# Kernel optimization log

Measured on AMD Instinct MI355X. Metric: run time of the kernel, lower is better.

## Reference

```python
import jax, jax.numpy as jnp
import numpy as np

W_WIN = 5  # sliding rank-pooling window (init arg w)
GRAY_W = np.array([0.2989, 0.587, 0.114], dtype=np.float32)  # torchvision Grayscale


def _window_weight_matrix(T, w):
    # Wmat[t, s] = rank-pooling weight of frame s inside window starting at t.
    # Window t covers frames t..t+N-1 with N = min(w, T-t); weights 2*(j+1)-N-1.
    M = np.zeros((T, T), dtype=np.float32)
    for t in range(T):
        N = min(w, T - t)
        for j in range(N):
            M[t, t + j] = 2.0 * (j + 1) - N - 1
    return jnp.asarray(M)


def setup_inputs() -> dict:
    key = jax.random.key(0)
    x = jax.random.normal(key, (8, 3, 64, 224, 224), dtype=jnp.float32)
    return {"x": x}


def reference(x):
    B, C, T, H, W = x.shape
    Wmat = _window_weight_matrix(T, W_WIN)  # [T, T], banded (bandwidth W_WIN)
    # Weighted sum over each sliding window: re[t] = sum_s Wmat[t,s] * x[:,:,s]
    re = jnp.einsum('ts,bcshw->tbchw', Wmat, x)  # [T,B,C,H,W]
    re = jax.nn.gelu(re, approximate=False)  # torch F.gelu is exact (erf)
    # Global (over B,C,H,W) min-subtract then max-normalize, per window t
    mn = re.min(axis=(1, 2, 3, 4), keepdims=True)
    re = re - mn
    mx = re.max(axis=(1, 2, 3, 4), keepdims=True)
    denom = jnp.where(mx != 0, mx, mx + 1e-5)
    re = re / denom
    # Grayscale: ITU-R 601 weighted channel sum -> 1 channel
    gray = jnp.einsum('tbchw,c->tbhw', re, jnp.asarray(GRAY_W, re.dtype))
    out = jnp.transpose(gray, (1, 0, 2, 3))[:, None]  # [B,1,T,H,W]
    mask = jnp.zeros((B, 1, W_WIN - 1, H, W), dtype=out.dtype)
    return jnp.concatenate([mask, out], axis=2)  # [B,1,T+w-1,H,W]
```

## Files before the change

### kernel.cpp

```cpp
#include <hip/hip_runtime.h>

#define HW 50176
#define HW2 25088
#define HW4 12544
#define TT 64
#define NB1 3136
#define NB3 3808
#define SUMW 0.9999f

__device__ __forceinline__ float gelu_erf(float x) {
    return 0.5f * x * (1.0f + erff(0.70710678f * x));
}
__device__ __forceinline__ float fast_rcp(float v) {
    float r; asm("v_rcp_f32 %0, %1" : "=v"(r) : "v"(v)); return r;
}
__device__ __forceinline__ float gelu_fast(float x) {
    float x2 = x * x;
    float e = exp2f(-x * fmaf(0.1029433f, x2, 2.3022078f));
    return x * fast_rcp(1.0f + e);
}
__device__ __forceinline__ unsigned encf(float f) {
    unsigned u = __float_as_uint(f);
    return (u & 0x80000000u) ? ~u : (u | 0x80000000u);
}
__device__ __forceinline__ float decf(unsigned u) {
    unsigned b = (u & 0x80000000u) ? (u ^ 0x80000000u) : ~u;
    return __uint_as_float(b);
}
__device__ __forceinline__ unsigned pk_min_f16(unsigned a, unsigned b) {
    unsigned r; asm("v_pk_min_f16 %0, %1, %2" : "=v"(r) : "v"(a), "v"(b)); return r;
}
__device__ __forceinline__ unsigned pack2(float lo, float hi) {
    auto p = __builtin_amdgcn_cvt_pkrtz(lo, hi);
    return __builtin_bit_cast(unsigned, p);
}
__device__ __forceinline__ unsigned mm2(float2 r) {
    return pk_min_f16(pack2(r.x, -r.x), pack2(r.y, -r.y));
}
__device__ __forceinline__ float2 re_full2(float2 w0, float2 w1, float2 w3, float2 w4) {
    float2 r;
    r.x = fmaf(4.f, w4.x - w0.x, 2.f * (w3.x - w1.x));
    r.y = fmaf(4.f, w4.y - w0.y, 2.f * (w3.y - w1.y));
    return r;
}

template<bool WGS>
__global__ __launch_bounds__(256, 6) void k_pass1(const float* __restrict__ x,
                                                  unsigned* __restrict__ gmm,
                                                  unsigned* __restrict__ gs) {
    __shared__ unsigned smin[16], smax[16];
    const int tid = threadIdx.x;
    if (tid < 16) { smin[tid] = 0xFFFFFFFFu; smax[tid] = 0u; }
    __syncthreads();

    const int bid = blockIdx.x;
    const int b   = bid / 392;
    const int rem = bid - b * 392;
    const int tc  = rem / 98;
    const int hwb = rem - tc * 98;
    const int t0  = tc * 16;
    const int hw  = (hwb * 256 + tid) * 2;
    const float* xa = x + ((size_t)(b * 3 + 0) * TT + t0) * (size_t)HW + hw;
    const float* xb = x + ((size_t)(b * 3 + 1) * TT + t0) * (size_t)HW + hw;
    const float* xc = x + ((size_t)(b * 3 + 2) * TT + t0) * (size_t)HW + hw;
    unsigned* gp = gs + ((size_t)b * TT + t0) * (size_t)HW2 + (hwb * 256 + tid);

    unsigned acc[16];
    #pragma unroll
    for (int j = 0; j < 16; ++j) acc[j] = 0x7BFF7BFFu;

    #define LDA(f) (*(const float2*)(xa + (size_t)(f) * HW))
    #define LDB(f) (*(const float2*)(xb + (size_t)(f) * HW))
    #define LDC(f) (*(const float2*)(xc + (size_t)(f) * HW))

    auto step = [&](float2 ra, float2 rb, float2 rc, int j) {
        acc[j] = pk_min_f16(acc[j], pk_min_f16(pk_min_f16(mm2(ra), mm2(rb)), mm2(rc)));
        if constexpr (WGS) {
            float gx = fmaf(0.114f, gelu_fast(rc.x), fmaf(0.587f, gelu_fast(rb.x), 0.2989f * gelu_fast(ra.x)));
            float gy = fmaf(0.114f, gelu_fast(rc.y), fmaf(0.587f, gelu_fast(rb.y), 0.2989f * gelu_fast(ra.y)));
            gp[(size_t)j * HW2] = pack2(gx, gy);
        }
    };

    float2 a0 = LDA(0), a1 = LDA(1), a2 = LDA(2), a3 = LDA(3), a4 = LDA(4), pa = LDA(5);
    float2 b0 = LDB(0), b1 = LDB(1), b2 = LDB(2), b3 = LDB(3), b4 = LDB(4), pb = LDB(5);
    float2 c0 = LDC(0), c1 = LDC(1), c2 = LDC(2), c3 = LDC(3), c4 = LDC(4), pc = LDC(5);

    if (tc < 3) {
        #pragma unroll
        for (int j = 0; j < 16; ++j) {
            step(re_full2(a0, a1, a3, a4), re_full2(b0, b1, b3, b4), re_full2(c0, c1, c3, c4), j);
            a0 = a1; a1 = a2; a2 = a3; a3 = a4; a4 = pa;
            b0 = b1; b1 = b2; b2 = b3; b3 = b4; b4 = pb;
            c0 = c1; c1 = c2; c2 = c3; c3 = c4; c4 = pc;
            if (j < 14) { pa = LDA(j + 6); pb = LDB(j + 6); pc = LDC(j + 6); }
        }
    } else {
        #pragma unroll
        for (int j = 0; j < 16; ++j) {
            float2 ra, rb, rc;
            if (j < 12) {
                ra = re_full2(a0, a1, a3, a4); rb = re_full2(b0, b1, b3, b4); rc = re_full2(c0, c1, c3, c4);
            } else if (j == 12) {
                ra.x = fmaf(3.f, a3.x - a0.x, a2.x - a1.x); ra.y = fmaf(3.f, a3.y - a0.y, a2.y - a1.y);
                rb.x = fmaf(3.f, b3.x - b0.x, b2.x - b1.x); rb.y = fmaf(3.f, b3.y - b0.y, b2.y - b1.y);
                rc.x = fmaf(3.f, c3.x - c0.x, c2.x - c1.x); rc.y = fmaf(3.f, c3.y - c0.y, c2.y - c1.y);
            } else if (j == 13) {
                ra.x = 2.f*(a2.x-a0.x); ra.y = 2.f*(a2.y-a0.y);
                rb.x = 2.f*(b2.x-b0.x); rb.y = 2.f*(b2.y-b0.y);
                rc.x = 2.f*(c2.x-c0.x); rc.y = 2.f*(c2.y-c0.y);
            } else if (j == 14) {
                ra.x = a1.x-a0.x; ra.y = a1.y-a0.y;
                rb.x = b1.x-b0.x; rb.y = b1.y-b0.y;
                rc.x = c1.x-c0.x; rc.y = c1.y-c0.y;
            } else {
                ra.x = ra.y = 0.f; rb = ra; rc = ra;
            }
            step(ra, rb, rc, j);
            a0 = a1; a1 = a2; a2 = a3; a3 = a4; a4 = pa;
            b0 = b1; b1 = b2; b2 = b3; b3 = b4; b4 = pb;
            c0 = c1; c1 = c2; c2 = c3; c3 = c4; c4 = pc;
            if (j < 10) { pa = LDA(j + 6); pb = LDB(j + 6); pc = LDC(j + 6); }
        }
    }
    #undef LDA
    #undef LDB
    #undef LDC

    const int lane = tid & 63;
    unsigned keep = 0x7BFF7BFFu;
    #pragma unroll
    for (int j = 0; j < 16; ++j) {
        unsigned a = acc[j];
        #pragma unroll
        for (int off = 32; off; off >>= 1)
            a = pk_min_f16(a, (unsigned)__shfl_xor((int)a, off, 64));
        if (lane == j) keep = a;
    }

    if (lane < 16) {
        union { unsigned u; _Float16 h[2]; } cv; cv.u = keep;
        const float amin = (float)cv.h[0];
        const float amax = -(float)cv.h[1];
        const float g0 = gelu_erf(amin), g1 = gelu_erf(amax);
        const float gmax = fmaxf(g0, g1);
        const float XSTAR = -0.7517916f;
        float gmin;
        if (amin >= XSTAR)      gmin = g0;
        else if (amax <= XSTAR) gmin = g1;
        else                    gmin = fminf(gelu_erf(XSTAR), fminf(g0, g1));
        atomicMin(&smin[lane], encf(gmin));
        atomicMax(&smax[lane], encf(gmax));
    }
    __syncthreads();
    if (tid < 16)            atomicMin(&gmm[t0 + tid], smin[tid]);
    else if (tid < 32)       atomicMax(&gmm[TT + t0 + tid - 16], smax[tid - 16]);
}

__global__ __launch_bounds__(256) void k_pass3(const unsigned* __restrict__ gs,
                                               const unsigned* __restrict__ gmm,
                                               float* __restrict__ out) {
    const int bid = blockIdx.x;
    const int b   = bid / 476;
    const int r   = bid - b * 476;
    const int t   = r / 7;
    const int seg = r - t * 7;
    const int base4 = seg * 1792 + threadIdx.x;
    float4* op = (float4*)out + ((size_t)b * 68 + t) * HW4 + base4;

    if (t < 4) {
        float4 z = make_float4(0.f, 0.f, 0.f, 0.f);
        #pragma unroll
        for (int k = 0; k < 7; ++k) op[k * 256] = z;
        return;
    }
    const int tm = t - 4;
    const float mn = decf(gmm[tm]);
    const float mx = decf(gmm[TT + tm]) - mn;
    const float inv = fast_rcp((mx != 0.f) ? mx : 1e-5f);
    const float A = inv, Bv = -mn * SUMW * inv;

    const uint2* gpp = (const uint2*)gs + ((size_t)b * TT + tm) * HW4 + base4;
    #pragma unroll
    for (int k = 0; k < 7; ++k) {
        uint2 v = gpp[k * 256];
        union { unsigned u; _Float16 h[2]; } lo, hi; lo.u = v.x; hi.u = v.y;
        float4 o;
        o.x = fmaf((float)lo.h[0], A, Bv);
        o.y = fmaf((float)lo.h[1], A, Bv);
        o.z = fmaf((float)hi.h[0], A, Bv);
        o.w = fmaf((float)hi.h[1], A, Bv);
        op[k * 256] = o;
    }
}

__global__ void k_consts(const unsigned* __restrict__ gmm, float* __restrict__ ab) {
    int t = threadIdx.x;
    float mn = decf(gmm[t]);
    float mx = decf(gmm[TT + t]) - mn;
    float inv = 1.0f / ((mx != 0.0f) ? mx : 1e-5f);
    ab[t]      = inv;
    ab[TT + t] = -mn * SUMW * inv;
}

__global__ __launch_bounds__(256) void k_pass2_direct(const float* __restrict__ x,
                                                      const float* __restrict__ ab,
                                                      float* __restrict__ out) {
    __shared__ float sA[TT], sB[TT];
    const int tid = threadIdx.x;
    if (tid < TT)          sA[tid] = ab[tid];
    else if (tid < 2 * TT) sB[tid - TT] = ab[tid];
    __syncthreads();

    const int pix = blockIdx.x * 256 + tid;
    const int b  = pix / HW;
    const int hw = pix - b * HW;
    const float* x0 = x + (size_t)(b * 3) * (TT * (size_t)HW) + hw;
    const float* x1 = x0 + (size_t)TT * HW;
    const float* x2 = x1 + (size_t)TT * HW;
    float* op = out + (size_t)b * (68 * (size_t)HW) + hw;

    op[0] = 0.f; op[HW] = 0.f; op[2 * (size_t)HW] = 0.f; op[3 * (size_t)HW] = 0.f;
    op += 4 * (size_t)HW;

    float a0 = x0[0], a1 = x0[HW], a2 = x0[2*HW], a3 = x0[3*HW], a4 = x0[4*HW];
    float b0 = x1[0], b1 = x1[HW], b2 = x1[2*HW], b3 = x1[3*HW], b4 = x1[4*HW];
    float c0 = x2[0], c1 = x2[HW], c2 = x2[2*HW], c3 = x2[3*HW], c4 = x2[4*HW];

    auto emit = [&](int t, float ra, float rb, float rc) {
        float gsv = 0.2989f * gelu_erf(ra) + 0.587f * gelu_erf(rb) + 0.114f * gelu_erf(rc);
        op[(size_t)t * HW] = fmaf(gsv, sA[t], sB[t]);
    };

    for (int t = 0; t < 59; ++t) {
        emit(t, 4.f*(a4-a0) + 2.f*(a3-a1), 4.f*(b4-b0) + 2.f*(b3-b1), 4.f*(c4-c0) + 2.f*(c3-c1));
        a0=a1; a1=a2; a2=a3; a3=a4; a4 = x0[(size_t)(t+5)*HW];
        b0=b1; b1=b2; b2=b3; b3=b4; b4 = x1[(size_t)(t+5)*HW];
        c0=c1; c1=c2; c2=c3; c3=c4; c4 = x2[(size_t)(t+5)*HW];
    }
    emit(59, 4.f*(a4-a0) + 2.f*(a3-a1), 4.f*(b4-b0) + 2.f*(b3-b1), 4.f*(c4-c0) + 2.f*(c3-c1));
    a0=a1; a1=a2; a2=a3; a3=a4; b0=b1; b1=b2; b2=b3; b3=b4; c0=c1; c1=c2; c2=c3; c3=c4;
    emit(60, 3.f*(a3-a0) + (a2-a1), 3.f*(b3-b0) + (b2-b1), 3.f*(c3-c0) + (c2-c1));
    a0=a1; a1=a2; a2=a3; b0=b1; b1=b2; b2=b3; c0=c1; c1=c2; c2=c3;
    emit(61, 2.f*(a2-a0), 2.f*(b2-b0), 2.f*(c2-c0));
    a0=a1; a1=a2; b0=b1; b1=b2; c0=c1; c1=c2;
    emit(62, a1-a0, b1-b0, c1-c0);
    op[63 * (size_t)HW] = sB[63];
}

extern "C" void kernel_launch(void* const* d_in, const int* in_sizes, int n_in,
                              void* d_out, int out_size, void* d_ws, size_t ws_size,
                              hipStream_t stream) {
    const float* x = (const float*)d_in[0];
    float* out = (float*)d_out;
    unsigned* gmm = (unsigned*)d_ws;
    float* ab = (float*)d_ws + 128;
    unsigned* gs = (unsigned*)((char*)d_ws + 1024);
    const size_t need = 1024 + (size_t)8 * TT * (size_t)HW * 2;

    hipMemsetAsync(gmm, 0xFF, TT * sizeof(unsigned), stream);
    hipMemsetAsync(gmm + TT, 0x00, TT * sizeof(unsigned), stream);

    if (ws_size >= need) {
        k_pass1<true><<<NB1, 256, 0, stream>>>(x, gmm, gs);
        k_pass3<<<NB3, 256, 0, stream>>>(gs, gmm, out);
    } else {
        k_pass1<false><<<NB1, 256, 0, stream>>>(x, gmm, nullptr);
        k_consts<<<1, 64, 0, stream>>>(gmm, ab);
        k_pass2_direct<<<1568, 256, 0, stream>>>(x, ab, out);
    }
}
```

Baseline: 132.5 us.

## Process full time axis per thread with scalar pixels to remove halo reloads

```diff
diff --git a/kernel.cpp b/kernel.cpp
--- a/kernel.cpp
+++ b/kernel.cpp
@@ -1,10 +1,9 @@
 #include <hip/hip_runtime.h>
 
 #define HW 50176
-#define HW2 25088
 #define HW4 12544
 #define TT 64
-#define NB1 3136
+#define NB1 1568
 #define NB3 3808
 #define SUMW 0.9999f
 
@@ -34,127 +33,105 @@
     auto p = __builtin_amdgcn_cvt_pkrtz(lo, hi);
     return __builtin_bit_cast(unsigned, p);
 }
-__device__ __forceinline__ unsigned mm2(float2 r) {
-    return pk_min_f16(pack2(r.x, -r.x), pack2(r.y, -r.y));
-}
-__device__ __forceinline__ float2 re_full2(float2 w0, float2 w1, float2 w3, float2 w4) {
-    float2 r;
-    r.x = fmaf(4.f, w4.x - w0.x, 2.f * (w3.x - w1.x));
-    r.y = fmaf(4.f, w4.y - w0.y, 2.f * (w3.y - w1.y));
-    return r;
+__device__ __forceinline__ unsigned pk2(float r) {
+    return pack2(r, -r);
 }
 
 template<bool WGS>
 __global__ __launch_bounds__(256, 6) void k_pass1(const float* __restrict__ x,
                                                   unsigned* __restrict__ gmm,
-                                                  unsigned* __restrict__ gs) {
-    __shared__ unsigned smin[16], smax[16];
+                                                  _Float16* __restrict__ gs) {
+    __shared__ unsigned smin[TT], smax[TT];
     const int tid = threadIdx.x;
-    if (tid < 16) { smin[tid] = 0xFFFFFFFFu; smax[tid] = 0u; }
+    if (tid < TT) { smin[tid] = 0xFFFFFFFFu; smax[tid] = 0u; }
     __syncthreads();
 
-    const int bid = blockIdx.x;
-    const int b   = bid / 392;
-    const int rem = bid - b * 392;
-    const int tc  = rem / 98;
-    const int hwb = rem - tc * 98;
-    const int t0  = tc * 16;
-    const int hw  = (hwb * 256 + tid) * 2;
-    const float* xa = x + ((size_t)(b * 3 + 0) * TT + t0) * (size_t)HW + hw;
-    const float* xb = x + ((size_t)(b * 3 + 1) * TT + t0) * (size_t)HW + hw;
-    const float* xc = x + ((size_t)(b * 3 + 2) * TT + t0) * (size_t)HW + hw;
-    unsigned* gp = gs + ((size_t)b * TT + t0) * (size_t)HW2 + (hwb * 256 + tid);
-
-    unsigned acc[16];
+    const int gid = blockIdx.x * 256 + tid;
+    const int b   = gid / HW;
+    const int hw  = gid - b * HW;
+    const float* xa = x + ((size_t)(b * 3 + 0) * TT) * (size_t)HW + hw;
+    const float* xb = x + ((size_t)(b * 3 + 1) * TT) * (size_t)HW + hw;
+    const float* xc = x + ((size_t)(b * 3 + 2) * TT) * (size_t)HW + hw;
+    _Float16* gp = gs + ((size_t)b * TT) * (size_t)HW + hw;
+
+    #define LA(f) xa[(size_t)(f) * HW]
+    #define LB(f) xb[(size_t)(f) * HW]
+    #define LC(f) xc[(size_t)(f) * HW]
+
+    float a0 = LA(0), a1 = LA(1), a2 = LA(2), a3 = LA(3), a4 = LA(4), pa = LA(5), qa = LA(6);
+    float b0 = LB(0), b1 = LB(1), b2 = LB(2), b3 = LB(3), b4 = LB(4), pb = LB(5), qb = LB(6);
+    float c0 = LC(0), c1 = LC(1), c2 = LC(2), c3 = LC(3), c4 = LC(4), pc = LC(5), qc = LC(6);
+
+    const int lane = tid & 63;
+
     #pragma unroll
-    for (int j = 0; j < 16; ++j) acc[j] = 0x7BFF7BFFu;
-
-    #define LDA(f) (*(const float2*)(xa + (size_t)(f) * HW))
-    #define LDB(f) (*(const float2*)(xb + (size_t)(f) * HW))
-    #define LDC(f) (*(const float2*)(xc + (size_t)(f) * HW))
-
-    auto step = [&](float2 ra, float2 rb, float2 rc, int j) {
-        acc[j] = pk_min_f16(acc[j], pk_min_f16(pk_min_f16(mm2(ra), mm2(rb)), mm2(rc)));
-        if constexpr (WGS) {
-            float gx = fmaf(0.114f, gelu_fast(rc.x), fmaf(0.587f, gelu_fast(rb.x), 0.2989f * gelu_fast(ra.x)));
-            float gy = fmaf(0.114f, gelu_fast(rc.y), fmaf(0.587f, gelu_fast(rb.y), 0.2989f * gelu_fast(ra.y)));
-            gp[(size_t)j * HW2] = pack2(gx, gy);
+    for (int seg = 0; seg < 4; ++seg) {
+        unsigned acc[16];
+        #pragma unroll
+        for (int j = 0; j < 16; ++j) acc[j] = 0x7BFF7BFFu;
+
+        #pragma unroll
+        for (int j = 0; j < 16; ++j) {
+            const int t = seg * 16 + j;
+            float ra, rb, rc;
+            if (t < 60) {
+                ra = fmaf(4.f, a4 - a0, 2.f * (a3 - a1));
+                rb = fmaf(4.f, b4 - b0, 2.f * (b3 - b1));
+                rc = fmaf(4.f, c4 - c0, 2.f * (c3 - c1));
+            } else if (t == 60) {
+                ra = fmaf(3.f, a3 - a0, a2 - a1);
+                rb = fmaf(3.f, b3 - b0, b2 - b1);
+                rc = fmaf(3.f, c3 - c0, c2 - c1);
+            } else if (t == 61) {
+                ra = 2.f * (a2 - a0); rb = 2.f * (b2 - b0); rc = 2.f * (c2 - c0);
+            } else if (t == 62) {
+                ra = a1 - a0; rb = b1 - b0; rc = c1 - c0;
+            } else {
+                ra = rb = rc = 0.f;
+            }
+            acc[j] = pk_min_f16(acc[j], pk_min_f16(pk_min_f16(pk2(ra), pk2(rb)), pk2(rc)));
+            if constexpr (WGS) {
+                float g = fmaf(0.114f, gelu_fast(rc),
+                          fmaf(0.587f, gelu_fast(rb), 0.2989f * gelu_fast(ra)));
+                gp[(size_t)t * HW] = (_Float16)g;
+            }
+            a0 = a1; a1 = a2; a2 = a3; a3 = a4; a4 = pa; pa = qa;
+            b0 = b1; b1 = b2; b2 = b3; b3 = b4; b4 = pb; pb = qb;
+            c0 = c1; c1 = c2; c2 = c3; c3 = c4; c4 = pc; pc = qc;
+            if (t < 57) { qa = LA(t + 7); qb = LB(t + 7); qc = LC(t + 7); }
         }
-    };
-
-    float2 a0 = LDA(0), a1 = LDA(1), a2 = LDA(2), a3 = LDA(3), a4 = LDA(4), pa = LDA(5);
-    float2 b0 = LDB(0), b1 = LDB(1), b2 = LDB(2), b3 = LDB(3), b4 = LDB(4), pb = LDB(5);
-    float2 c0 = LDC(0), c1 = LDC(1), c2 = LDC(2), c3 = LDC(3), c4 = LDC(4), pc = LDC(5);
-
-    if (tc < 3) {
+
+        unsigned keep = 0x7BFF7BFFu;
         #pragma unroll
         for (int j = 0; j < 16; ++j) {
-            step(re_full2(a0, a1, a3, a4), re_full2(b0, b1, b3, b4), re_full2(c0, c1, c3, c4), j);
-            a0 = a1; a1 = a2; a2 = a3; a3 = a4; a4 = pa;
-            b0 = b1; b1 = b2; b2 = b3; b3 = b4; b4 = pb;
-            c0 = c1; c1 = c2; c2 = c3; c3 = c4; c4 = pc;
-            if (j < 14) { pa = LDA(j + 6); pb = LDB(j + 6); pc = LDC(j + 6); }
+            unsigned a = acc[j];
+            #pragma unroll
+            for (int off = 32; off; off >>= 1)
+                a = pk_min_f16(a, (unsigned)__shfl_xor((int)a, off, 64));
+            if (lane == j) keep = a;
         }
-    } else {
-        #pragma unroll
-        for (int j = 0; j < 16; ++j) {
-            float2 ra, rb, rc;
-            if (j < 12) {
-                ra = re_full2(a0, a1, a3, a4); rb = re_full2(b0, b1, b3, b4); rc = re_full2(c0, c1, c3, c4);
-            } else if (j == 12) {
-                ra.x = fmaf(3.f, a3.x - a0.x, a2.x - a1.x); ra.y = fmaf(3.f, a3.y - a0.y, a2.y - a1.y);
-                rb.x = fmaf(3.f, b3.x - b0.x, b2.x - b1.x); rb.y = fmaf(3.f, b3.y - b0.y, b2.y - b1.y);
-                rc.x = fmaf(3.f, c3.x - c0.x, c2.x - c1.x); rc.y = fmaf(3.f, c3.y - c0.y, c2.y - c1.y);
-            } else if (j == 13) {
-                ra.x = 2.f*(a2.x-a0.x); ra.y = 2.f*(a2.y-a0.y);
-                rb.x = 2.f*(b2.x-b0.x); rb.y = 2.f*(b2.y-b0.y);
-                rc.x = 2.f*(c2.x-c0.x); rc.y = 2.f*(c2.y-c0.y);
-            } else if (j == 14) {
-                ra.x = a1.x-a0.x; ra.y = a1.y-a0.y;
-                rb.x = b1.x-b0.x; rb.y = b1.y-b0.y;
-                rc.x = c1.x-c0.x; rc.y = c1.y-c0.y;
-            } else {
-                ra.x = ra.y = 0.f; rb = ra; rc = ra;
-            }
-            step(ra, rb, rc, j);
-            a0 = a1; a1 = a2; a2 = a3; a3 = a4; a4 = pa;
-            b0 = b1; b1 = b2; b2 = b3; b3 = b4; b4 = pb;
-            c0 = c1; c1 = c2; c2 = c3; c3 = c4; c4 = pc;
-            if (j < 10) { pa = LDA(j + 6); pb = LDB(j + 6); pc = LDC(j + 6); }
+        if (lane < 16) {
+            union { unsigned u; _Float16 h[2]; } cv; cv.u = keep;
+            const float amin = (float)cv.h[0];
+            const float amax = -(float)cv.h[1];
+            const float g0 = gelu_erf(amin), g1 = gelu_erf(amax);
+            const float gmax = fmaxf(g0, g1);
+            const float XSTAR = -0.7517916f;
+            float gmin;
+            if (amin >= XSTAR)      gmin = g0;
+            else if (amax <= XSTAR) gmin = g1;
+            else                    gmin = fminf(gelu_erf(XSTAR), fminf(g0, g1));
+            atomicMin(&smin[seg * 16 + lane], encf(gmin));
+            atomicMax(&smax[seg * 16 + lane], encf(gmax));
         }
     }
-    #undef LDA
-    #undef LDB
-    #undef LDC
-
-    const int lane = tid & 63;
-    unsigned keep = 0x7BFF7BFFu;
-    #pragma unroll
-    for (int j = 0; j < 16; ++j) {
-        unsigned a = acc[j];
-        #pragma unroll
-        for (int off = 32; off; off >>= 1)
-            a = pk_min_f16(a, (unsigned)__shfl_xor((int)a, off, 64));
-        if (lane == j) keep = a;
-    }
-
-    if (lane < 16) {
-        union { unsigned u; _Float16 h[2]; } cv; cv.u = keep;
-        const float amin = (float)cv.h[0];
-        const float amax = -(float)cv.h[1];
-        const float g0 = gelu_erf(amin), g1 = gelu_erf(amax);
-        const float gmax = fmaxf(g0, g1);
-        const float XSTAR = -0.7517916f;
-        float gmin;
-        if (amin >= XSTAR)      gmin = g0;
-        else if (amax <= XSTAR) gmin = g1;
-        else                    gmin = fminf(gelu_erf(XSTAR), fminf(g0, g1));
-        atomicMin(&smin[lane], encf(gmin));
-        atomicMax(&smax[lane], encf(gmax));
-    }
+    #undef LA
+    #undef LB
+    #undef LC
+
     __syncthreads();
-    if (tid < 16)            atomicMin(&gmm[t0 + tid], smin[tid]);
-    else if (tid < 32)       atomicMax(&gmm[TT + t0 + tid - 16], smax[tid - 16]);
+    if (tid < TT)            atomicMin(&gmm[tid], smin[tid]);
+    else if (tid < 2 * TT)   atomicMax(&gmm[TT + tid - TT], smax[tid - TT]);
 }
 
 __global__ __launch_bounds__(256) void k_pass3(const unsigned* __restrict__ gs,
@@ -255,7 +232,7 @@
     float* out = (float*)d_out;
     unsigned* gmm = (unsigned*)d_ws;
     float* ab = (float*)d_ws + 128;
-    unsigned* gs = (unsigned*)((char*)d_ws + 1024);
+    _Float16* gs = (_Float16*)((char*)d_ws + 1024);
     const size_t need = 1024 + (size_t)8 * TT * (size_t)HW * 2;
 
     hipMemsetAsync(gmm, 0xFF, TT * sizeof(unsigned), stream);
@@ -263,7 +240,7 @@
 
     if (ws_size >= need) {
         k_pass1<true><<<NB1, 256, 0, stream>>>(x, gmm, gs);
-        k_pass3<<<NB3, 256, 0, stream>>>(gs, gmm, out);
+        k_pass3<<<NB3, 256, 0, stream>>>((const unsigned*)gs, gmm, out);
     } else {
         k_pass1<false><<<NB1, 256, 0, stream>>>(x, gmm, nullptr);
         k_consts<<<1, 64, 0, stream>>>(gmm, ab);
```

Result: no change. 134.6 us (+1.6%).

## Fuse min/max pass and normalize pass into one cooperative kernel with register-held grayscale

Applied to the files above, without the earlier changes.

```diff
diff --git a/kernel.cpp b/kernel.cpp
--- a/kernel.cpp
+++ b/kernel.cpp
@@ -1,11 +1,12 @@
 #include <hip/hip_runtime.h>
+#include <hip/hip_cooperative_groups.h>
+
+namespace cg = cooperative_groups;
 
 #define HW 50176
 #define HW2 25088
 #define HW4 12544
 #define TT 64
-#define NB1 3136
-#define NB3 3808
 #define SUMW 0.9999f
 
 __device__ __forceinline__ float gelu_erf(float x) {
@@ -34,14 +35,145 @@
     auto p = __builtin_amdgcn_cvt_pkrtz(lo, hi);
     return __builtin_bit_cast(unsigned, p);
 }
+__device__ __forceinline__ unsigned pk2(float r) { return pack2(r, -r); }
 __device__ __forceinline__ unsigned mm2(float2 r) {
-    return pk_min_f16(pack2(r.x, -r.x), pack2(r.y, -r.y));
+    return pk_min_f16(pk2(r.x), pk2(r.y));
 }
 __device__ __forceinline__ float2 re_full2(float2 w0, float2 w1, float2 w3, float2 w4) {
     float2 r;
     r.x = fmaf(4.f, w4.x - w0.x, 2.f * (w3.x - w1.x));
     r.y = fmaf(4.f, w4.y - w0.y, 2.f * (w3.y - w1.y));
     return r;
+}
+
+__global__ __launch_bounds__(256, 7) void k_fused(const float* __restrict__ x,
+                                                  unsigned* __restrict__ gmm,
+                                                  float* __restrict__ out) {
+    __shared__ unsigned smin[TT], smax[TT];
+    __shared__ float sA[TT], sB[TT];
+    const int tid = threadIdx.x;
+    if (tid < TT) smin[tid] = 0xFFFFFFFFu;
+    else if (tid < 2 * TT) smax[tid - TT] = 0u;
+    __syncthreads();
+
+    const int px = blockIdx.x * 256 + tid;
+    const int b  = px / HW;
+    const int hw = px - b * HW;
+    const float* xa = x + ((size_t)(b * 3 + 0) * TT) * (size_t)HW + hw;
+    const float* xb = x + ((size_t)(b * 3 + 1) * TT) * (size_t)HW + hw;
+    const float* xc = x + ((size_t)(b * 3 + 2) * TT) * (size_t)HW + hw;
+
+    unsigned G0,G1,G2,G3,G4,G5,G6,G7,G8,G9,G10,G11,G12,G13,G14,G15,
+             G16,G17,G18,G19,G20,G21,G22,G23,G24,G25,G26,G27,G28,G29,G30,G31;
+    #define GREG(i) (i==0?G0:i==1?G1:i==2?G2:i==3?G3:i==4?G4:i==5?G5:i==6?G6:i==7?G7: \
+                     i==8?G8:i==9?G9:i==10?G10:i==11?G11:i==12?G12:i==13?G13:i==14?G14:i==15?G15: \
+                     i==16?G16:i==17?G17:i==18?G18:i==19?G19:i==20?G20:i==21?G21:i==22?G22:i==23?G23: \
+                     i==24?G24:i==25?G25:i==26?G26:i==27?G27:i==28?G28:i==29?G29:i==30?G30:G31)
+    unsigned A0,A1,A2,A3,A4,A5,A6,A7;
+    #define ACC(j) (j==0?A0:j==1?A1:j==2?A2:j==3?A3:j==4?A4:j==5?A5:j==6?A6:A7)
+
+    float a0 = xa[0], a1 = xa[HW], a2 = xa[2*(size_t)HW], a3 = xa[3*(size_t)HW], a4 = xa[4*(size_t)HW], pa = xa[5*(size_t)HW];
+    float b0 = xb[0], b1 = xb[HW], b2 = xb[2*(size_t)HW], b3 = xb[3*(size_t)HW], b4 = xb[4*(size_t)HW], pb = xb[5*(size_t)HW];
+    float c0 = xc[0], c1 = xc[HW], c2 = xc[2*(size_t)HW], c3 = xc[3*(size_t)HW], c4 = xc[4*(size_t)HW], pc = xc[5*(size_t)HW];
+
+    const int lane = tid & 63;
+    float gprev = 0.f;
+
+    #pragma unroll
+    for (int g = 0; g < 8; ++g) {
+        A0=A1=A2=A3=A4=A5=A6=A7=0x7BFF7BFFu;
+
+        #pragma unroll
+        for (int j = 0; j < 8; ++j) {
+            const int t = g * 8 + j;
+            float ra, rb, rc;
+            if (t < 60) {
+                ra = fmaf(4.f, a4 - a0, 2.f * (a3 - a1));
+                rb = fmaf(4.f, b4 - b0, 2.f * (b3 - b1));
+                rc = fmaf(4.f, c4 - c0, 2.f * (c3 - c1));
+            } else if (t == 60) {
+                ra = fmaf(3.f, a3 - a0, a2 - a1);
+                rb = fmaf(3.f, b3 - b0, b2 - b1);
+                rc = fmaf(3.f, c3 - c0, c2 - c1);
+            } else if (t == 61) {
+                ra = 2.f * (a2 - a0); rb = 2.f * (b2 - b0); rc = 2.f * (c2 - c0);
+            } else if (t == 62) {
+                ra = a1 - a0; rb = b1 - b0; rc = c1 - c0;
+            } else {
+                ra = rb = rc = 0.f;
+            }
+            ACC(j) = pk_min_f16(ACC(j), pk_min_f16(pk_min_f16(pk2(ra), pk2(rb)), pk2(rc)));
+            float gg = fmaf(0.114f, gelu_fast(rc),
+                       fmaf(0.587f, gelu_fast(rb), 0.2989f * gelu_fast(ra)));
+            if (t & 1) GREG(t >> 1) = pack2(gprev, gg);
+            else       gprev = gg;
+            a0=a1; a1=a2; a2=a3; a3=a4; a4=pa;
+            b0=b1; b1=b2; b2=b3; b3=b4; b4=pb;
+            c0=c1; c1=c2; c2=c3; c3=c4; c4=pc;
+            if (t < 58) {
+                pa = xa[(size_t)(t + 6) * HW];
+                pb = xb[(size_t)(t + 6) * HW];
+                pc = xc[(size_t)(t + 6) * HW];
+            }
+        }
+
+        unsigned keep = 0x7BFF7BFFu;
+        #define BFLY(A, J) { unsigned v = A; \
+            v = pk_min_f16(v, (unsigned)__shfl_xor((int)v, 32, 64)); \
+            v = pk_min_f16(v, (unsigned)__shfl_xor((int)v, 16, 64)); \
+            v = pk_min_f16(v, (unsigned)__shfl_xor((int)v,  8, 64)); \
+            v = pk_min_f16(v, (unsigned)__shfl_xor((int)v,  4, 64)); \
+            v = pk_min_f16(v, (unsigned)__shfl_xor((int)v,  2, 64)); \
+            v = pk_min_f16(v, (unsigned)__shfl_xor((int)v,  1, 64)); \
+            if (lane == (J)) keep = v; }
+        BFLY(A0,0) BFLY(A1,1) BFLY(A2,2) BFLY(A3,3)
+        BFLY(A4,4) BFLY(A5,5) BFLY(A6,6) BFLY(A7,7)
+        #undef BFLY
+
+        if (lane < 8) {
+            union { unsigned u; _Float16 h[2]; } cv; cv.u = keep;
+            const float amin = (float)cv.h[0];
+            const float amax = -(float)cv.h[1];
+            const float g0 = gelu_erf(amin), g1 = gelu_erf(amax);
+            const float gmax = fmaxf(g0, g1);
+            const float XSTAR = -0.7517916f;
+            float gmin;
+            if (amin >= XSTAR)      gmin = g0;
+            else if (amax <= XSTAR) gmin = g1;
+            else                    gmin = fminf(gelu_erf(XSTAR), fminf(g0, g1));
+            atomicMin(&smin[g * 8 + lane], encf(gmin));
+            atomicMax(&smax[g * 8 + lane], encf(gmax));
+        }
+    }
+    #undef ACC
+
+    __syncthreads();
+    if (tid < TT)            atomicMin(&gmm[tid], smin[tid]);
+    else if (tid < 2 * TT)   atomicMax(&gmm[TT + tid - TT], smax[tid - TT]);
+
+    cg::this_grid().sync();
+
+    if (tid < TT) {
+        unsigned mnu = __hip_atomic_load(&gmm[tid],      __ATOMIC_RELAXED, __HIP_MEMORY_SCOPE_AGENT);
+        unsigned mxu = __hip_atomic_load(&gmm[TT + tid], __ATOMIC_RELAXED, __HIP_MEMORY_SCOPE_AGENT);
+        float mn = decf(mnu);
+        float mx = decf(mxu) - mn;
+        float inv = fast_rcp((mx != 0.f) ? mx : 1e-5f);
+        sA[tid] = inv;
+        sB[tid] = -mn * SUMW * inv;
+    }
+    __syncthreads();
+
+    float* op = out + (size_t)b * (68 * (size_t)HW) + hw;
+    op[0] = 0.f; op[HW] = 0.f; op[2 * (size_t)HW] = 0.f; op[3 * (size_t)HW] = 0.f;
+    op += 4 * (size_t)HW;
+    #pragma unroll
+    for (int i = 0; i < 32; ++i) {
+        union { unsigned u; _Float16 h[2]; } cv; cv.u = GREG(i);
+        op[(size_t)(2 * i)     * HW] = fmaf((float)cv.h[0], sA[2 * i],     sB[2 * i]);
+        op[(size_t)(2 * i + 1) * HW] = fmaf((float)cv.h[1], sA[2 * i + 1], sB[2 * i + 1]);
+    }
+    #undef GREG
 }
 
 template<bool WGS>
@@ -261,12 +393,29 @@
     hipMemsetAsync(gmm, 0xFF, TT * sizeof(unsigned), stream);
     hipMemsetAsync(gmm + TT, 0x00, TT * sizeof(unsigned), stream);
 
-    if (ws_size >= need) {
-        k_pass1<true><<<NB1, 256, 0, stream>>>(x, gmm, gs);
-        k_pass3<<<NB3, 256, 0, stream>>>(gs, gmm, out);
-    } else {
-        k_pass1<false><<<NB1, 256, 0, stream>>>(x, gmm, nullptr);
-        k_consts<<<1, 64, 0, stream>>>(gmm, ab);
-        k_pass2_direct<<<1568, 256, 0, stream>>>(x, ab, out);
-    }
-}
+    bool coop_done = false;
+    int dev = 0;
+    (void)hipGetDevice(&dev);
+    int ncu = 0;
+    (void)hipDeviceGetAttribute(&ncu, hipDeviceAttributeMultiprocessorCount, dev);
+    int maxb = 0;
+    (void)hipOccupancyMaxActiveBlocksPerMultiprocessor(&maxb, k_fused, 256, 0);
+    if ((long long)maxb * (long long)ncu >= 1568LL) {
+        void* args[] = { (void*)&x, (void*)&gmm, (void*)&out };
+        hipError_t e = hipLaunchCooperativeKernel((void*)k_fused, dim3(1568), dim3(256),
+                                                  args, 0, stream);
+        if (e == hipSuccess) coop_done = true;
+        else (void)hipGetLastError();
+    }
+
+    if (!coop_done) {
+        if (ws_size >= need) {
+            k_pass1<true><<<3136, 256, 0, stream>>>(x, gmm, gs);
+            k_pass3<<<3808, 256, 0, stream>>>(gs, gmm, out);
+        } else {
+            k_pass1<false><<<3136, 256, 0, stream>>>(x, gmm, nullptr);
+            k_consts<<<1, 64, 0, stream>>>(gmm, ab);
+            k_pass2_direct<<<1568, 256, 0, stream>>>(x, ab, out);
+        }
+    }
+}
```

New measurement: 132.6 us. Within noise of the previous version (+0.0%).

## Process all 64 frames per block in pass1 to remove halo reloads

Applied to the files above, without the earlier changes.

```diff
diff --git a/kernel.cpp b/kernel.cpp
--- a/kernel.cpp
+++ b/kernel.cpp
@@ -4,8 +4,6 @@
 #define HW2 25088
 #define HW4 12544
 #define TT 64
-#define NB1 3136
-#define NB3 3808
 #define SUMW 0.9999f
 
 __device__ __forceinline__ float gelu_erf(float x) {
@@ -34,111 +32,145 @@
     auto p = __builtin_amdgcn_cvt_pkrtz(lo, hi);
     return __builtin_bit_cast(unsigned, p);
 }
-__device__ __forceinline__ unsigned mm2(float2 r) {
-    return pk_min_f16(pack2(r.x, -r.x), pack2(r.y, -r.y));
-}
-__device__ __forceinline__ float2 re_full2(float2 w0, float2 w1, float2 w3, float2 w4) {
-    float2 r;
-    r.x = fmaf(4.f, w4.x - w0.x, 2.f * (w3.x - w1.x));
-    r.y = fmaf(4.f, w4.y - w0.y, 2.f * (w3.y - w1.y));
-    return r;
-}
+__device__ __forceinline__ unsigned pk2(float r) { return pack2(r, -r); }
+__device__ __forceinline__ unsigned mm2(float2 r) { return pk_min_f16(pk2(r.x), pk2(r.y)); }
 
 template<bool WGS>
-__global__ __launch_bounds__(256, 6) void k_pass1(const float* __restrict__ x,
+__global__ __launch_bounds__(256, 4) void k_pass1(const float* __restrict__ x,
                                                   unsigned* __restrict__ gmm,
                                                   unsigned* __restrict__ gs) {
-    __shared__ unsigned smin[16], smax[16];
+    __shared__ unsigned smin[TT], smax[TT];
     const int tid = threadIdx.x;
-    if (tid < 16) { smin[tid] = 0xFFFFFFFFu; smax[tid] = 0u; }
+    if (tid < TT) smin[tid] = 0xFFFFFFFFu;
+    else if (tid < 2 * TT) smax[tid - TT] = 0u;
     __syncthreads();
 
     const int bid = blockIdx.x;
-    const int b   = bid / 392;
-    const int rem = bid - b * 392;
-    const int tc  = rem / 98;
-    const int hwb = rem - tc * 98;
-    const int t0  = tc * 16;
+    const int b   = bid / 98;
+    const int hwb = bid - b * 98;
     const int hw  = (hwb * 256 + tid) * 2;
-    const float* xa = x + ((size_t)(b * 3 + 0) * TT + t0) * (size_t)HW + hw;
-    const float* xb = x + ((size_t)(b * 3 + 1) * TT + t0) * (size_t)HW + hw;
-    const float* xc = x + ((size_t)(b * 3 + 2) * TT + t0) * (size_t)HW + hw;
-    unsigned* gp = gs + ((size_t)b * TT + t0) * (size_t)HW2 + (hwb * 256 + tid);
-
-    unsigned acc[16];
-    #pragma unroll
-    for (int j = 0; j < 16; ++j) acc[j] = 0x7BFF7BFFu;
-
-    #define LDA(f) (*(const float2*)(xa + (size_t)(f) * HW))
-    #define LDB(f) (*(const float2*)(xb + (size_t)(f) * HW))
-    #define LDC(f) (*(const float2*)(xc + (size_t)(f) * HW))
-
-    auto step = [&](float2 ra, float2 rb, float2 rc, int j) {
-        acc[j] = pk_min_f16(acc[j], pk_min_f16(pk_min_f16(mm2(ra), mm2(rb)), mm2(rc)));
-        if constexpr (WGS) {
-            float gx = fmaf(0.114f, gelu_fast(rc.x), fmaf(0.587f, gelu_fast(rb.x), 0.2989f * gelu_fast(ra.x)));
-            float gy = fmaf(0.114f, gelu_fast(rc.y), fmaf(0.587f, gelu_fast(rb.y), 0.2989f * gelu_fast(ra.y)));
-            gp[(size_t)j * HW2] = pack2(gx, gy);
-        }
-    };
-
-    float2 a0 = LDA(0), a1 = LDA(1), a2 = LDA(2), a3 = LDA(3), a4 = LDA(4), pa = LDA(5);
-    float2 b0 = LDB(0), b1 = LDB(1), b2 = LDB(2), b3 = LDB(3), b4 = LDB(4), pb = LDB(5);
-    float2 c0 = LDC(0), c1 = LDC(1), c2 = LDC(2), c3 = LDC(3), c4 = LDC(4), pc = LDC(5);
-
-    if (tc < 3) {
-        #pragma unroll
-        for (int j = 0; j < 16; ++j) {
-            step(re_full2(a0, a1, a3, a4), re_full2(b0, b1, b3, b4), re_full2(c0, c1, c3, c4), j);
-            a0 = a1; a1 = a2; a2 = a3; a3 = a4; a4 = pa;
-            b0 = b1; b1 = b2; b2 = b3; b3 = b4; b4 = pb;
-            c0 = c1; c1 = c2; c2 = c3; c3 = c4; c4 = pc;
-            if (j < 14) { pa = LDA(j + 6); pb = LDB(j + 6); pc = LDC(j + 6); }
-        }
-    } else {
-        #pragma unroll
-        for (int j = 0; j < 16; ++j) {
-            float2 ra, rb, rc;
-            if (j < 12) {
-                ra = re_full2(a0, a1, a3, a4); rb = re_full2(b0, b1, b3, b4); rc = re_full2(c0, c1, c3, c4);
-            } else if (j == 12) {
-                ra.x = fmaf(3.f, a3.x - a0.x, a2.x - a1.x); ra.y = fmaf(3.f, a3.y - a0.y, a2.y - a1.y);
-                rb.x = fmaf(3.f, b3.x - b0.x, b2.x - b1.x); rb.y = fmaf(3.f, b3.y - b0.y, b2.y - b1.y);
-                rc.x = fmaf(3.f, c3.x - c0.x, c2.x - c1.x); rc.y = fmaf(3.f, c3.y - c0.y, c2.y - c1.y);
-            } else if (j == 13) {
-                ra.x = 2.f*(a2.x-a0.x); ra.y = 2.f*(a2.y-a0.y);
-                rb.x = 2.f*(b2.x-b0.x); rb.y = 2.f*(b2.y-b0.y);
-                rc.x = 2.f*(c2.x-c0.x); rc.y = 2.f*(c2.y-c0.y);
-            } else if (j == 14) {
-                ra.x = a1.x-a0.x; ra.y = a1.y-a0.y;
-                rb.x = b1.x-b0.x; rb.y = b1.y-b0.y;
-                rc.x = c1.x-c0.x; rc.y = c1.y-c0.y;
-            } else {
-                ra.x = ra.y = 0.f; rb = ra; rc = ra;
-            }
-            step(ra, rb, rc, j);
-            a0 = a1; a1 = a2; a2 = a3; a3 = a4; a4 = pa;
-            b0 = b1; b1 = b2; b2 = b3; b3 = b4; b4 = pb;
-            c0 = c1; c1 = c2; c2 = c3; c3 = c4; c4 = pc;
-            if (j < 10) { pa = LDA(j + 6); pb = LDB(j + 6); pc = LDC(j + 6); }
-        }
-    }
-    #undef LDA
-    #undef LDB
-    #undef LDC
+    const float* xa = x + ((size_t)(b * 3 + 0) * TT) * (size_t)HW + hw;
+    const float* xb = x + ((size_t)(b * 3 + 1) * TT) * (size_t)HW + hw;
+    const float* xc = x + ((size_t)(b * 3 + 2) * TT) * (size_t)HW + hw;
+    unsigned* gp = gs + ((size_t)b * TT) * (size_t)HW2 + (hwb * 256 + tid);
 
     const int lane = tid & 63;
     unsigned keep = 0x7BFF7BFFu;
-    #pragma unroll
-    for (int j = 0; j < 16; ++j) {
-        unsigned a = acc[j];
-        #pragma unroll
-        for (int off = 32; off; off >>= 1)
-            a = pk_min_f16(a, (unsigned)__shfl_xor((int)a, off, 64));
-        if (lane == j) keep = a;
-    }
-
-    if (lane < 16) {
+
+    float2 a0 = *(const float2*)xa, b0 = *(const float2*)xb, c0 = *(const float2*)xc;
+    float2 a1 = *(const float2*)(xa + HW), b1 = *(const float2*)(xb + HW), c1 = *(const float2*)(xc + HW);
+    float2 a2 = *(const float2*)(xa + 2*(size_t)HW), b2 = *(const float2*)(xb + 2*(size_t)HW), c2 = *(const float2*)(xc + 2*(size_t)HW);
+    float2 a3 = *(const float2*)(xa + 3*(size_t)HW), b3 = *(const float2*)(xb + 3*(size_t)HW), c3 = *(const float2*)(xc + 3*(size_t)HW);
+    float2 a4 = *(const float2*)(xa + 4*(size_t)HW), b4 = *(const float2*)(xb + 4*(size_t)HW), c4 = *(const float2*)(xc + 4*(size_t)HW);
+    float2 pa = *(const float2*)(xa + 5*(size_t)HW), pb = *(const float2*)(xb + 5*(size_t)HW), pc = *(const float2*)(xc + 5*(size_t)HW);
+    xa += 6 * (size_t)HW; xb += 6 * (size_t)HW; xc += 6 * (size_t)HW;
+
+    unsigned acc[8];
+
+    #define STEP_FULL(J) { \
+        float2 ra, rb, rc; \
+        ra.x = fmaf(4.f, a4.x - a0.x, 2.f * (a3.x - a1.x)); ra.y = fmaf(4.f, a4.y - a0.y, 2.f * (a3.y - a1.y)); \
+        rb.x = fmaf(4.f, b4.x - b0.x, 2.f * (b3.x - b1.x)); rb.y = fmaf(4.f, b4.y - b0.y, 2.f * (b3.y - b1.y)); \
+        rc.x = fmaf(4.f, c4.x - c0.x, 2.f * (c3.x - c1.x)); rc.y = fmaf(4.f, c4.y - c0.y, 2.f * (c3.y - c1.y)); \
+        acc[J] = pk_min_f16(acc[J], pk_min_f16(pk_min_f16(mm2(ra), mm2(rb)), mm2(rc))); \
+        if constexpr (WGS) { \
+            float gx = fmaf(0.114f, gelu_fast(rc.x), fmaf(0.587f, gelu_fast(rb.x), 0.2989f * gelu_fast(ra.x))); \
+            float gy = fmaf(0.114f, gelu_fast(rc.y), fmaf(0.587f, gelu_fast(rb.y), 0.2989f * gelu_fast(ra.y))); \
+            *gp = pack2(gx, gy); \
+        } \
+        gp += HW2; \
+        a0 = a1; a1 = a2; a2 = a3; a3 = a4; a4 = pa; \
+        b0 = b1; b1 = b2; b2 = b3; b3 = b4; b4 = pb; \
+        c0 = c1; c1 = c2; c2 = c3; c3 = c4; c4 = pc; }
+
+    #define PREFETCH() { pa = *(const float2*)xa; pb = *(const float2*)xb; pc = *(const float2*)xc; \
+                         xa += HW; xb += HW; xc += HW; }
+
+    #define FLUSH(J, T) { unsigned v = acc[J]; \
+        v = pk_min_f16(v, (unsigned)__shfl_xor((int)v, 32, 64)); \
+        v = pk_min_f16(v, (unsigned)__shfl_xor((int)v, 16, 64)); \
+        v = pk_min_f16(v, (unsigned)__shfl_xor((int)v,  8, 64)); \
+        v = pk_min_f16(v, (unsigned)__shfl_xor((int)v,  4, 64)); \
+        v = pk_min_f16(v, (unsigned)__shfl_xor((int)v,  2, 64)); \
+        v = pk_min_f16(v, (unsigned)__shfl_xor((int)v,  1, 64)); \
+        if (lane == (T)) keep = v; }
+
+    for (int g = 0; g < 7; ++g) {
+        #pragma unroll
+        for (int j = 0; j < 8; ++j) acc[j] = 0x7BFF7BFFu;
+        #pragma unroll
+        for (int j = 0; j < 8; ++j) {
+            STEP_FULL(j)
+            PREFETCH()
+        }
+        #pragma unroll
+        for (int j = 0; j < 8; ++j) FLUSH(j, g * 8 + j)
+    }
+
+    {
+        #pragma unroll
+        for (int j = 0; j < 8; ++j) acc[j] = 0x7BFF7BFFu;
+        STEP_FULL(0) PREFETCH()
+        STEP_FULL(1) PREFETCH()
+        STEP_FULL(2)
+        STEP_FULL(3)
+        {
+            float2 ra, rb, rc;
+            ra.x = fmaf(3.f, a3.x - a0.x, a2.x - a1.x); ra.y = fmaf(3.f, a3.y - a0.y, a2.y - a1.y);
+            rb.x = fmaf(3.f, b3.x - b0.x, b2.x - b1.x); rb.y = fmaf(3.f, b3.y - b0.y, b2.y - b1.y);
+            rc.x = fmaf(3.f, c3.x - c0.x, c2.x - c1.x); rc.y = fmaf(3.f, c3.y - c0.y, c2.y - c1.y);
+            acc[4] = pk_min_f16(acc[4], pk_min_f16(pk_min_f16(mm2(ra), mm2(rb)), mm2(rc)));
+            if constexpr (WGS) {
+                float gx = fmaf(0.114f, gelu_fast(rc.x), fmaf(0.587f, gelu_fast(rb.x), 0.2989f * gelu_fast(ra.x)));
+                float gy = fmaf(0.114f, gelu_fast(rc.y), fmaf(0.587f, gelu_fast(rb.y), 0.2989f * gelu_fast(ra.y)));
+                *gp = pack2(gx, gy);
+            }
+            gp += HW2;
+            a0 = a1; a1 = a2; a2 = a3;
+            b0 = b1; b1 = b2; b2 = b3;
+            c0 = c1; c1 = c2; c2 = c3;
+        }
+        {
+            float2 ra, rb, rc;
+            ra.x = 2.f*(a2.x-a0.x); ra.y = 2.f*(a2.y-a0.y);
+            rb.x = 2.f*(b2.x-b0.x); rb.y = 2.f*(b2.y-b0.y);
+            rc.x = 2.f*(c2.x-c0.x); rc.y = 2.f*(c2.y-c0.y);
+            acc[5] = pk_min_f16(acc[5], pk_min_f16(pk_min_f16(mm2(ra), mm2(rb)), mm2(rc)));
+            if constexpr (WGS) {
+                float gx = fmaf(0.114f, gelu_fast(rc.x), fmaf(0.587f, gelu_fast(rb.x), 0.2989f * gelu_fast(ra.x)));
+                float gy = fmaf(0.114f, gelu_fast(rc.y), fmaf(0.587f, gelu_fast(rb.y), 0.2989f * gelu_fast(ra.y)));
+                *gp = pack2(gx, gy);
+            }
+            gp += HW2;
+            a0 = a1; a1 = a2;
+            b0 = b1; b1 = b2;
+            c0 = c1; c1 = c2;
+        }
+        {
+            float2 ra, rb, rc;
+            ra.x = a1.x-a0.x; ra.y = a1.y-a0.y;
+            rb.x = b1.x-b0.x; rb.y = b1.y-b0.y;
+            rc.x = c1.x-c0.x; rc.y = c1.y-c0.y;
+            acc[6] = pk_min_f16(acc[6], pk_min_f16(pk_min_f16(mm2(ra), mm2(rb)), mm2(rc)));
+            if constexpr (WGS) {
+                float gx = fmaf(0.114f, gelu_fast(rc.x), fmaf(0.587f, gelu_fast(rb.x), 0.2989f * gelu_fast(ra.x)));
+                float gy = fmaf(0.114f, gelu_fast(rc.y), fmaf(0.587f, gelu_fast(rb.y), 0.2989f * gelu_fast(ra.y)));
+                *gp = pack2(gx, gy);
+            }
+            gp += HW2;
+        }
+        {
+            acc[7] = pk_min_f16(acc[7], 0u);
+            if constexpr (WGS) *gp = 0u;
+        }
+        #pragma unroll
+        for (int j = 0; j < 8; ++j) FLUSH(j, 56 + j)
+    }
+    #undef STEP_FULL
+    #undef PREFETCH
+    #undef FLUSH
+
+    {
         union { unsigned u; _Float16 h[2]; } cv; cv.u = keep;
         const float amin = (float)cv.h[0];
         const float amax = -(float)cv.h[1];
@@ -153,8 +185,8 @@
         atomicMax(&smax[lane], encf(gmax));
     }
     __syncthreads();
-    if (tid < 16)            atomicMin(&gmm[t0 + tid], smin[tid]);
-    else if (tid < 32)       atomicMax(&gmm[TT + t0 + tid - 16], smax[tid - 16]);
+    if (tid < TT)            atomicMin(&gmm[tid], smin[tid]);
+    else if (tid < 2 * TT)   atomicMax(&gmm[TT + tid - TT], smax[tid - TT]);
 }
 
 __global__ __launch_bounds__(256) void k_pass3(const unsigned* __restrict__ gs,
@@ -262,10 +294,10 @@
     hipMemsetAsync(gmm + TT, 0x00, TT * sizeof(unsigned), stream);
 
     if (ws_size >= need) {
-        k_pass1<true><<<NB1, 256, 0, stream>>>(x, gmm, gs);
-        k_pass3<<<NB3, 256, 0, stream>>>(gs, gmm, out);
+        k_pass1<true><<<784, 256, 0, stream>>>(x, gmm, gs);
+        k_pass3<<<3808, 256, 0, stream>>>(gs, gmm, out);
     } else {
-        k_pass1<false><<<NB1, 256, 0, stream>>>(x, gmm, nullptr);
+        k_pass1<false><<<784, 256, 0, stream>>>(x, gmm, nullptr);
         k_consts<<<1, 64, 0, stream>>>(gmm, ab);
         k_pass2_direct<<<1568, 256, 0, stream>>>(x, ab, out);
     }
```

Result: no change. 132.0 us (-0.4%).
